# Performance work log

Hardware: AMD Instinct MI355X
Metric: run time of the kernel (lower is better)

## Reference

```python
import jax, jax.numpy as jnp
import numpy as np

_HMT = np.array([[1, 1, 1, 1], [1, -1, 1, -1], [1, 1, -1, -1], [1, -1, -1, 1]], dtype=np.float32)
_H = jnp.asarray(_HMT)
_H2 = jnp.asarray(_HMT[[1, 0, 2, 3], :])
_H3 = jnp.asarray(_HMT[[3, 1, 2, 0], :])
# inverse-transform rows 1:3 (2x4), reconstructed from truncated source
_IH = _H[1:3, :]
_IH2 = _H2[1:3, :]
_IH3 = _H3[1:3, :]

KERNEL = 4
STRIDE = 2


def setup_inputs() -> dict:
    key = jax.random.key(0)
    k1, k2, k3 = jax.random.split(key, 3)
    B, Cin, Cout, ih, iw = 16, 64, 96, 128, 128
    x = jax.random.normal(k1, (B, Cin, ih, iw), dtype=jnp.float32)
    weight = jax.random.normal(k2, (Cout, Cin, KERNEL, KERNEL), dtype=jnp.float32) * 0.05
    bias = jax.random.normal(k3, (1, Cout, 1, 1), dtype=jnp.float32) * 0.05
    return {"x": x, "weight": weight, "bias": bias}


def _extract_patches(xp, nH, nW):
    # patches[b,c,i,j,u,v] = xp[b,c, 2i+v, 2j+u]  (torch unfold(3).unfold(2) order)
    idx_h = 2 * np.arange(nH)[:, None] + np.arange(KERNEL)[None, :]  # (nH,4) over (i,v)
    idx_w = 2 * np.arange(nW)[:, None] + np.arange(KERNEL)[None, :]  # (nW,4) over (j,u)
    return xp[:, :, idx_h[:, None, None, :], idx_w[None, :, :, None]]  # (B,C,nH,nW,4,4)


def _group(t, w, ih_mat):
    # t: (B,C,nH,nW,4,4) transform-domain patches; w: (Og,C,4,4)
    m = jnp.einsum('bcijuv,ocuv->boijuv', t, w)
    # IH @ m @ IH.T -> (B,Og,nH,nW,2,2)
    return jnp.einsum('pu,boijuv,qv->boijpq', ih_mat, m, ih_mat)


def reference(x, weight, bias):
    B, Cin, ih, iw = x.shape
    Cout = weight.shape[0]
    nH, nW = ih // STRIDE, iw // STRIDE
    xp = jnp.pad(x, ((0, 0), (0, 0), (1, 1), (1, 1)))
    patches = _extract_patches(xp, nH, nW)
    # forward transforms: H @ P @ H ; H2.T @ P @ H2 ; H3.T @ P @ H3
    t1 = jnp.einsum('au,bcijuv,vd->bcijad', _H, patches, _H)
    t2 = jnp.einsum('ua,bcijuv,vd->bcijad', _H2, patches, _H2)
    t3 = jnp.einsum('ua,bcijuv,vd->bcijad', _H3, patches, _H3)
    g = Cout // 3
    h1 = _group(t1, weight[:g], _IH)
    h2 = _group(t2, weight[g:2 * g], _IH2)
    h3 = _group(t3, weight[2 * g:], _IH3)
    hmult = jnp.concatenate([h1, h2, h3], axis=1)  # (B,Cout,nH,nW,2,2)
    # out[b,o,2i+p,2j+q] = hmult[b,o,i,j,p,q]
    out = hmult.transpose(0, 1, 2, 4, 3, 5).reshape(B, Cout, ih, iw)
    return out + bias
```

## Files before the change

### kernel.cpp

```cpp
#include <hip/hip_runtime.h>
#include <hip/hip_bf16.h>
#include <cstddef>
#include <cstdint>


#define IHW 128
#define CIN 64
#define COUT 96
#define NCK 32
#define XB_DW 816
#define AB_DW 2048

typedef __attribute__((ext_vector_type(8))) short short8_t;
typedef __attribute__((ext_vector_type(4))) float floatx4;

__device__ __forceinline__ short bf16r(float f) {
  uint32_t u = __float_as_uint(f);
  uint32_t r = (u + 0x7FFFu + ((u >> 16) & 1u)) >> 16;
  return (short)r;
}

__device__ __forceinline__ uint32_t pk(float lo, float hi) {
  union { __hip_bfloat16 h; unsigned short s; } a, bq;
  a.h = __float2bfloat16(lo);
  bq.h = __float2bfloat16(hi);
  return (uint32_t)a.s | ((uint32_t)bq.s << 16);
}

__global__ __launch_bounds__(256) void prep_all(const float* __restrict__ x,
                                                const float* __restrict__ w,
                                                uint32_t* __restrict__ img,
                                                short* __restrict__ keff,
                                                int do_img) {
  if (blockIdx.x < 24) {
    int idx = blockIdx.x * 256 + threadIdx.x;
    if (idx >= COUT * CIN) return;
    int o = idx / CIN, c = idx % CIN;
    int g = o / 32;

    int perm[4] = {0, 1, 2, 3};
    if (g == 1) { perm[0] = 1; perm[1] = 0; }
    else if (g == 2) { perm[0] = 3; perm[3] = 0; }

    const float H[4][4] = {{1,1,1,1},{1,-1,1,-1},{1,1,-1,-1},{1,-1,-1,1}};
    float S[2][4];
#pragma unroll
    for (int p = 0; p < 2; ++p)
#pragma unroll
      for (int a = 0; a < 4; ++a) {
        bool pos = (g == 1) ? ((p == 0) ? true : (a < 2))
                            : ((p == 0) ? ((a & 1) == 0) : (a < 2));
        S[p][a] = pos ? 1.f : -1.f;
      }

    float wv[4][4];
#pragma unroll
    for (int a = 0; a < 4; ++a)
#pragma unroll
      for (int d = 0; d < 4; ++d) wv[a][d] = w[(o * CIN + c) * 16 + a * 4 + d];

    for (int p = 0; p < 2; ++p)
      for (int q = 0; q < 2; ++q) {
        int n = o * 4 + p * 2 + q;
        for (int y = 0; y < 4; ++y)
          for (int xx = 0; xx < 4; ++xx) {
            float s = 0.f;
#pragma unroll
            for (int a = 0; a < 4; ++a) {
              float ea = S[p][a] * H[a][perm[xx]];
#pragma unroll
              for (int d = 0; d < 4; ++d) s += ea * S[q][d] * H[d][perm[y]] * wv[a][d];
            }
            keff[n * 1024 + c * 16 + y * 4 + xx] = bf16r(s);
          }
      }
    return;
  }
  if (!do_img) return;

  const int t = (blockIdx.x - 24) * 256 + threadIdx.x;
  const int r = t >> 5;
  const int l = t & 31;
  const int py = r % 130;
  const int rc = r / 130;

  uint32_t d0 = 0, d1 = 0, t0 = 0;
  if (py != 0 && py != 129) {
    const float4 v = *reinterpret_cast<const float4*>(
        x + ((size_t)rc * IHW + (py - 1)) * IHW + 4 * l);
    float prev = __shfl_up(v.w, 1, 32);
    if (l == 0) prev = 0.f;
    d0 = pk(prev, v.x);
    d1 = pk(v.y, v.z);
    t0 = pk(v.w, 0.f);
  }
  uint32_t* row = img + (size_t)r * 68;
  *reinterpret_cast<uint2*>(row + 2 * l) = make_uint2(d0, d1);
  if (l == 31) *reinterpret_cast<uint4*>(row + 64) = make_uint4(t0, 0, 0, 0);
}

__global__ __launch_bounds__(256) void conv_mfma(const uint32_t* __restrict__ img,
                                                 const short* __restrict__ keff,
                                                 const float* __restrict__ bias,
                                                 float* __restrict__ out) {
  __shared__ uint32_t alds[4 * AB_DW];
  __shared__ uint32_t xlds[4 * XB_DW];

  const int tid = threadIdx.x;
  const int lane = tid & 63;
  const int wid = tid >> 6;
  const int wavem = wid >> 1;
  const int wn = wid & 1;
  const int l15 = lane & 15;
  const int l4 = lane >> 4;

  const int hw = blockIdx.x;
  const int xcd = hw & 7;
  const int r = hw >> 3;
  const int tile = xcd * 64 + r / 3;
  const int nblk = r % 3;
  const int b = tile >> 5;
  const int ib = tile & 31;

  const uint32_t* imgb = img + (size_t)b * CIN * 130 * 68;

  int xsrc = 0;
  const bool xact = tid < 204;
  {
    const int ri = tid / 17;
    const int col16 = tid % 17;
    const int y = ri >> 1;
    const int cs = ri & 1;
    xsrc = (cs * 130 + 4 * ib + y) * 68 + col16 * 4;
  }

  int asrc[2];
#pragma unroll
  for (int it = 0; it < 2; ++it) {
    const int slot = tid + it * 256;
    const int n = slot >> 2;
    const int p = slot & 3;
    asrc[it] = (nblk * 128 + n) * 1024 + ((p ^ ((n >> 1) & 3)) << 3);
  }

#define STAGE(bs, ckv)                                                     \
  {                                                                        \
    _Pragma("unroll") for (int it = 0; it < 2; ++it) {                     \
      const short* src = keff + asrc[it] + (ckv) * 32;                     \
      __builtin_amdgcn_global_load_lds(                                    \
          (const __attribute__((address_space(1))) void*)src,              \
          (__attribute__((address_space(3))) void*)                        \
              &alds[(bs) * AB_DW + (tid + it * 256) * 4],                  \
          16, 0, 0);                                                       \
    }                                                                      \
    if (xact) {                                                            \
      const uint32_t* src = imgb + xsrc + (ckv) * (2 * 130 * 68);          \
      __builtin_amdgcn_global_load_lds(                                    \
          (const __attribute__((address_space(1))) void*)src,              \
          (__attribute__((address_space(3))) void*)                        \
              &xlds[(bs) * XB_DW + tid * 4],                               \
          16, 0, 0);                                                       \
    }                                                                      \
  }

  union ufrag { short8_t s8; uint32_t u[4]; };

  floatx4 acc[4][4];
#pragma unroll
  for (int i2 = 0; i2 < 4; ++i2)
#pragma unroll
    for (int j2 = 0; j2 < 4; ++j2) acc[i2][j2] = (floatx4){0.f, 0.f, 0.f, 0.f};

  float biasr[4];
#pragma unroll
  for (int nf = 0; nf < 4; ++nf) biasr[nf] = bias[nblk * 32 + wn * 16 + nf * 4 + l4];

  const int abase = (wn * 64 + l15) * 16 + ((l4 ^ ((l15 >> 1) & 3)) << 2);
  const int xbase = (4 * wavem + 4 * (l4 & 1) + (l4 >> 1)) * 68 + l15;

#define COMPUTE(ckv)                                                       \
  {                                                                        \
    const uint32_t* Ap = alds + ((ckv) & 3) * AB_DW;                       \
    const uint32_t* Xp = xlds + ((ckv) & 3) * XB_DW + xbase;               \
    short8_t af[4];                                                        \
    _Pragma("unroll") for (int nf = 0; nf < 4; ++nf)                       \
      af[nf] = *reinterpret_cast<const short8_t*>(Ap + abase + nf * 256);  \
    ufrag xf[4];                                                           \
    _Pragma("unroll") for (int mf = 0; mf < 4; ++mf) {                     \
      const int o = mf * 16;                                               \
      xf[mf].u[0] = Xp[o];                                                 \
      xf[mf].u[1] = Xp[o + 1];                                             \
      xf[mf].u[2] = Xp[o + 136];                                           \
      xf[mf].u[3] = Xp[o + 137];                                           \
    }                                                                      \
    _Pragma("unroll") for (int mf = 0; mf < 4; ++mf)                       \
      _Pragma("unroll") for (int nf = 0; nf < 4; ++nf)                     \
        acc[mf][nf] = __builtin_amdgcn_mfma_f32_16x16x32_bf16(             \
            af[nf], xf[mf].s8, acc[mf][nf], 0, 0, 0);                      \
  }

  STAGE(0, 0);
  __builtin_amdgcn_sched_barrier(0);
  STAGE(1, 1);
  __builtin_amdgcn_sched_barrier(0);

  for (int ck = 0; ck < NCK - 2; ++ck) {
    STAGE((ck + 2) & 3, ck + 2);
    asm volatile("s_waitcnt vmcnt(6)" ::: "memory");
    __builtin_amdgcn_s_barrier();
    __builtin_amdgcn_sched_barrier(0);
    COMPUTE(ck);
  }
  asm volatile("s_waitcnt vmcnt(3)" ::: "memory");
  __builtin_amdgcn_s_barrier();
  __builtin_amdgcn_sched_barrier(0);
  COMPUTE(NCK - 2);
  asm volatile("s_waitcnt vmcnt(0)" ::: "memory");
  __builtin_amdgcn_s_barrier();
  __builtin_amdgcn_sched_barrier(0);
  COMPUTE(NCK - 1);

  const int i_row = ib * 2 + wavem;
  const int orow0 = 2 * i_row;
#pragma unroll
  for (int nf = 0; nf < 4; ++nf) {
    const int o = nblk * 32 + wn * 16 + nf * 4 + l4;
    const float bv = biasr[nf];
    float* obase = out + ((size_t)(b * COUT + o) * IHW + orow0) * IHW;
#pragma unroll
    for (int mf = 0; mf < 4; ++mf) {
      const int col = 2 * (mf * 16 + l15);
      float2 s0 = make_float2(acc[mf][nf][0] + bv, acc[mf][nf][1] + bv);
      float2 s1 = make_float2(acc[mf][nf][2] + bv, acc[mf][nf][3] + bv);
      *reinterpret_cast<float2*>(obase + col) = s0;
      *reinterpret_cast<float2*>(obase + IHW + col) = s1;
    }
  }
#undef STAGE
#undef COMPUTE
}

#define FB_P_DW 168
#define FB_COFF 80
#define FB_XBUF (12 * FB_P_DW)
#define FB_ABUF 4096

__global__ __launch_bounds__(256) void conv_fb(const float* __restrict__ x,
                                               const short* __restrict__ keff,
                                               const float* __restrict__ bias,
                                               float* __restrict__ out) {
  __shared__ uint32_t xlds[2 * FB_XBUF];
  __shared__ uint32_t alds[2 * FB_ABUF];

  const int tid = threadIdx.x;
  const int lane = tid & 63;
  const int wid = tid >> 6;
  const int wavem = wid >> 1;
  const int wn = wid & 1;
  const int l15 = lane & 15;
  const int l4 = lane >> 4;

  const int hw = blockIdx.x;
  const int xcd = hw & 7;
  const int r = hw >> 3;
  const int tile = xcd * 64 + r / 3;
  const int nblk = r % 3;
  const int b = tile >> 5;
  const int ib = tile & 31;
  const int gy0 = ib * 4 - 1;

  const float* xb = x + (size_t)b * CIN * IHW * IHW;

  int sl_off[3], sl_dw[3], sl_s[3];
  bool sl_ok[3];
#pragma unroll
  for (int it = 0; it < 3; ++it) {
    const int slot = tid + it * 256;
    const int seg = slot >> 5;
    const int s = slot & 31;
    const int c_sub = seg / 12;
    const int rr = seg % 12;
    const int kk2 = rr / 6;
    const int y = rr % 6;
    const int c_loc = 2 * kk2 + c_sub;
    const int gy = gy0 + y;
    const bool ok = (unsigned)gy < (unsigned)IHW;
    sl_off[it] = (c_loc * IHW + (ok ? gy : 0)) * IHW + 4 * s;
    sl_dw[it] = rr * FB_P_DW + c_sub * FB_COFF;
    sl_s[it] = s;
    sl_ok[it] = ok;
  }

  int aoff[4];
#pragma unroll
  for (int it = 0; it < 4; ++it) {
    const int slot = tid + it * 256;
    const int n = slot >> 3;
    const int u = slot & 7;
    aoff[it] = (nblk * 128 + n) * 1024 + ((u ^ (n & 7)) << 3);
  }

  float4 gv[3];
  float gn[3];
#define FISSUE(ckv)                                                       \
  {                                                                       \
    _Pragma("unroll") for (int it = 0; it < 3; ++it) {                    \
      const float* p = xb + sl_off[it] + (size_t)(ckv) * (4 * IHW * IHW); \
      gv[it] = *reinterpret_cast<const float4*>(p);                       \
      gn[it] = (sl_s[it] < 31) ? p[4] : 0.f;                              \
    }                                                                     \
  }
#define FWRITE(bs)                                                        \
  {                                                                       \
    uint32_t* Bp = xlds + (bs) * FB_XBUF;                                 \
    _Pragma("unroll") for (int it = 0; it < 3; ++it) {                    \
      float4 v = gv[it];                                                  \
      float nx = gn[it];                                                  \
      if (!sl_ok[it]) { v.x = 0.f; v.y = 0.f; v.z = 0.f; v.w = 0.f; nx = 0.f; } \
      const int o = sl_dw[it] + 2 * sl_s[it] + 1;                         \
      Bp[o] = pk(v.y, v.z);                                               \
      Bp[o + 1] = pk(v.w, nx);                                            \
      if (sl_s[it] == 0) Bp[sl_dw[it]] = pk(0.f, v.x);                    \
    }                                                                     \
  }
#define FADMA(bs, ckv)                                                    \
  {                                                                       \
    _Pragma("unroll") for (int it = 0; it < 4; ++it) {                    \
      const short* src = keff + aoff[it] + (ckv) * 64;                    \
      __builtin_amdgcn_global_load_lds(                                   \
          (const __attribute__((address_space(1))) void*)src,             \
          (__attribute__((address_space(3))) void*)                       \
              &alds[(bs) * FB_ABUF + (tid + it * 256) * 4],               \
          16, 0, 0);                                                      \
    }                                                                     \
  }

  union ufragf { short8_t s8; uint32_t u[4]; };
#define FKK(Apt, Xkt, abasev)                                             \
  {                                                                       \
    short8_t af[4];                                                       \
    _Pragma("unroll") for (int nf = 0; nf < 4; ++nf)                      \
      af[nf] = *reinterpret_cast<const short8_t*>((Apt) + (abasev) + nf * 512); \
    ufragf xf[4];                                                         \
    _Pragma("unroll") for (int mf = 0; mf < 4; ++mf) {                    \
      xf[mf].u[0] = (Xkt)[mf * 16];                                       \
      xf[mf].u[1] = (Xkt)[mf * 16 + 1];                                   \
      xf[mf].u[2] = (Xkt)[mf * 16 + FB_P_DW];                             \
      xf[mf].u[3] = (Xkt)[mf * 16 + FB_P_DW + 1];                         \
    }                                                                     \
    _Pragma("unroll") for (int mf = 0; mf < 4; ++mf)                      \
      _Pragma("unroll") for (int nf = 0; nf < 4; ++nf)                    \
        acc[mf][nf] = __builtin_amdgcn_mfma_f32_16x16x32_bf16(            \
            af[nf], xf[mf].s8, acc[mf][nf], 0, 0, 0);                     \
  }

  floatx4 acc[4][4];
#pragma unroll
  for (int i2 = 0; i2 < 4; ++i2)
#pragma unroll
    for (int j2 = 0; j2 < 4; ++j2) acc[i2][j2] = (floatx4){0.f, 0.f, 0.f, 0.f};

  float biasr[4];
#pragma unroll
  for (int nf = 0; nf < 4; ++nf) biasr[nf] = bias[nblk * 32 + wn * 16 + nf * 4 + l4];

  const int cm_dw = (2 * wavem + 2 * (l4 & 1)) * FB_P_DW + (l4 >> 1) * FB_COFF + l15;
  const int a0 = (wn * 64 + l15) * 32 + ((l4 ^ (l15 & 7)) << 2);
  const int a1 = a0 ^ 16;

  FISSUE(0);
  FADMA(0, 0);
  FWRITE(0);
  FISSUE(1);

  for (int ck = 0; ck < 16 - 1; ++ck) {
    asm volatile("s_waitcnt vmcnt(6) lgkmcnt(0)" ::: "memory");
    __builtin_amdgcn_s_barrier();
    __builtin_amdgcn_sched_barrier(0);
    const int cur = ck & 1;
    const uint32_t* Ap = alds + cur * FB_ABUF;
    const uint32_t* Xk0 = xlds + cur * FB_XBUF + cm_dw;
    const uint32_t* Xk1 = Xk0 + 6 * FB_P_DW;
    FADMA(cur ^ 1, ck + 1);
    FKK(Ap, Xk0, a0);
    FKK(Ap, Xk1, a1);
    FWRITE(cur ^ 1);
    if (ck + 2 < 16) FISSUE(ck + 2);
  }
  asm volatile("s_waitcnt vmcnt(0) lgkmcnt(0)" ::: "memory");
  __builtin_amdgcn_s_barrier();
  __builtin_amdgcn_sched_barrier(0);
  {
    const uint32_t* Ap = alds + FB_ABUF;
    const uint32_t* Xk0 = xlds + FB_XBUF + cm_dw;
    const uint32_t* Xk1 = Xk0 + 6 * FB_P_DW;
    FKK(Ap, Xk0, a0);
    FKK(Ap, Xk1, a1);
  }

  const int i_row = ib * 2 + wavem;
  const int orow0 = 2 * i_row;
#pragma unroll
  for (int nf = 0; nf < 4; ++nf) {
    const int o = nblk * 32 + wn * 16 + nf * 4 + l4;
    const float bv = biasr[nf];
    float* obase = out + ((size_t)(b * COUT + o) * IHW + orow0) * IHW;
#pragma unroll
    for (int mf = 0; mf < 4; ++mf) {
      const int col = 2 * (mf * 16 + l15);
      float2 s0 = make_float2(acc[mf][nf][0] + bv, acc[mf][nf][1] + bv);
      float2 s1 = make_float2(acc[mf][nf][2] + bv, acc[mf][nf][3] + bv);
      *reinterpret_cast<float2*>(obase + col) = s0;
      *reinterpret_cast<float2*>(obase + IHW + col) = s1;
    }
  }
#undef FISSUE
#undef FWRITE
#undef FADMA
#undef FKK
}

extern "C" void kernel_launch(void* const* d_in, const int* in_sizes, int n_in,
                              void* d_out, int out_size, void* d_ws, size_t ws_size,
                              hipStream_t stream) {
  const float* x = (const float*)d_in[0];
  const float* w = (const float*)d_in[1];
  const float* bias = (const float*)d_in[2];
  float* out = (float*)d_out;
  short* keff = (short*)d_ws;
  uint32_t* img = (uint32_t*)((char*)d_ws + 786432);

  const size_t NEED = 786432 + (size_t)16 * 64 * 130 * 272;
  const bool big = ws_size >= NEED;

  hipLaunchKernelGGL(prep_all, dim3(big ? 16664 : 24), dim3(256), 0, stream,
                     x, w, img, keff, big ? 1 : 0);
  if (big) {
    hipLaunchKernelGGL(conv_mfma, dim3(1536), dim3(256), 0, stream, img, keff, bias, out);
  } else {
    hipLaunchKernelGGL(conv_fb, dim3(1536), dim3(256), 0, stream, x, keff, bias, out);
  }
}
```

Measured before the change: 86.15 us.

## Load weight fragments directly into registers with double-buffered prefetch

The weight (A) operand is no longer staged through LDS with async global-to-LDS copies. Each wave now loads its MFMA weight fragments straight from global memory into registers, alternating between two register buffers. The main loop is unrolled by two and the vmcnt waits are adjusted to the new per-stage load counts. This frees 32 KB of LDS per block and removes the LDS reads for A, which may raise occupancy. The cost is that waves sharing the same weights each fetch them separately, with strided, less coalesced global loads and higher register pressure.

```diff
diff --git a/kernel.cpp b/kernel.cpp
--- a/kernel.cpp
+++ b/kernel.cpp
@@ -9,7 +9,6 @@
 #define COUT 96
 #define NCK 32
 #define XB_DW 816
-#define AB_DW 2048
 
 typedef __attribute__((ext_vector_type(8))) short short8_t;
 typedef __attribute__((ext_vector_type(4))) float floatx4;
@@ -103,7 +102,6 @@
                                                  const short* __restrict__ keff,
                                                  const float* __restrict__ bias,
                                                  float* __restrict__ out) {
-  __shared__ uint32_t alds[4 * AB_DW];
   __shared__ uint32_t xlds[4 * XB_DW];
 
   const int tid = threadIdx.x;
@@ -134,25 +132,8 @@
     xsrc = (cs * 130 + 4 * ib + y) * 68 + col16 * 4;
   }
 
-  int asrc[2];
-#pragma unroll
-  for (int it = 0; it < 2; ++it) {
-    const int slot = tid + it * 256;
-    const int n = slot >> 2;
-    const int p = slot & 3;
-    asrc[it] = (nblk * 128 + n) * 1024 + ((p ^ ((n >> 1) & 3)) << 3);
-  }
-
-#define STAGE(bs, ckv)                                                     \
+#define XSTAGE(bs, ckv)                                                    \
   {                                                                        \
-    _Pragma("unroll") for (int it = 0; it < 2; ++it) {                     \
-      const short* src = keff + asrc[it] + (ckv) * 32;                     \
-      __builtin_amdgcn_global_load_lds(                                    \
-          (const __attribute__((address_space(1))) void*)src,              \
-          (__attribute__((address_space(3))) void*)                        \
-              &alds[(bs) * AB_DW + (tid + it * 256) * 4],                  \
-          16, 0, 0);                                                       \
-    }                                                                      \
     if (xact) {                                                            \
       const uint32_t* src = imgb + xsrc + (ckv) * (2 * 130 * 68);          \
       __builtin_amdgcn_global_load_lds(                                    \
@@ -163,6 +144,14 @@
     }                                                                      \
   }
 
+  const short* aptr = keff + ((size_t)(nblk * 128 + wn * 64 + l15)) * 1024 + l4 * 8;
+
+#define ALOAD(af, ckv)                                                     \
+  {                                                                        \
+    _Pragma("unroll") for (int nf = 0; nf < 4; ++nf)                       \
+      af[nf] = *reinterpret_cast<const short8_t*>(aptr + nf * 16384 + (ckv) * 32); \
+  }
+
   union ufrag { short8_t s8; uint32_t u[4]; };
 
   floatx4 acc[4][4];
@@ -175,16 +164,11 @@
 #pragma unroll
   for (int nf = 0; nf < 4; ++nf) biasr[nf] = bias[nblk * 32 + wn * 16 + nf * 4 + l4];
 
-  const int abase = (wn * 64 + l15) * 16 + ((l4 ^ ((l15 >> 1) & 3)) << 2);
   const int xbase = (4 * wavem + 4 * (l4 & 1) + (l4 >> 1)) * 68 + l15;
 
-#define COMPUTE(ckv)                                                       \
+#define COMPUTE(ckv, af)                                                   \
   {                                                                        \
-    const uint32_t* Ap = alds + ((ckv) & 3) * AB_DW;                       \
     const uint32_t* Xp = xlds + ((ckv) & 3) * XB_DW + xbase;               \
-    short8_t af[4];                                                        \
-    _Pragma("unroll") for (int nf = 0; nf < 4; ++nf)                       \
-      af[nf] = *reinterpret_cast<const short8_t*>(Ap + abase + nf * 256);  \
     ufrag xf[4];                                                           \
     _Pragma("unroll") for (int mf = 0; mf < 4; ++mf) {                     \
       const int o = mf * 16;                                               \
@@ -199,26 +183,45 @@
             af[nf], xf[mf].s8, acc[mf][nf], 0, 0, 0);                      \
   }
 
-  STAGE(0, 0);
-  __builtin_amdgcn_sched_barrier(0);
-  STAGE(1, 1);
-  __builtin_amdgcn_sched_barrier(0);
-
-  for (int ck = 0; ck < NCK - 2; ++ck) {
-    STAGE((ck + 2) & 3, ck + 2);
+  short8_t afA[4], afB[4];
+
+  XSTAGE(0, 0);
+  __builtin_amdgcn_sched_barrier(0);
+  ALOAD(afA, 0);
+  __builtin_amdgcn_sched_barrier(0);
+  XSTAGE(1, 1);
+  __builtin_amdgcn_sched_barrier(0);
+  ALOAD(afB, 1);
+  __builtin_amdgcn_sched_barrier(0);
+
+  for (int ck = 0; ck < NCK - 2; ck += 2) {
+    XSTAGE((ck + 2) & 3, ck + 2);
     asm volatile("s_waitcnt vmcnt(6)" ::: "memory");
     __builtin_amdgcn_s_barrier();
     __builtin_amdgcn_sched_barrier(0);
-    COMPUTE(ck);
-  }
-  asm volatile("s_waitcnt vmcnt(3)" ::: "memory");
+    COMPUTE(ck, afA);
+    __builtin_amdgcn_sched_barrier(0);
+    ALOAD(afA, ck + 2);
+    __builtin_amdgcn_sched_barrier(0);
+
+    XSTAGE((ck + 3) & 3, ck + 3);
+    asm volatile("s_waitcnt vmcnt(6)" ::: "memory");
+    __builtin_amdgcn_s_barrier();
+    __builtin_amdgcn_sched_barrier(0);
+    COMPUTE(ck + 1, afB);
+    __builtin_amdgcn_sched_barrier(0);
+    ALOAD(afB, ck + 3);
+    __builtin_amdgcn_sched_barrier(0);
+  }
+
+  asm volatile("s_waitcnt vmcnt(5)" ::: "memory");
   __builtin_amdgcn_s_barrier();
   __builtin_amdgcn_sched_barrier(0);
-  COMPUTE(NCK - 2);
+  COMPUTE(NCK - 2, afA);
   asm volatile("s_waitcnt vmcnt(0)" ::: "memory");
   __builtin_amdgcn_s_barrier();
   __builtin_amdgcn_sched_barrier(0);
-  COMPUTE(NCK - 1);
+  COMPUTE(NCK - 1, afB);
 
   const int i_row = ib * 2 + wavem;
   const int orow0 = 2 * i_row;
@@ -236,7 +239,8 @@
       *reinterpret_cast<float2*>(obase + IHW + col) = s1;
     }
   }
-#undef STAGE
+#undef XSTAGE
+#undef ALOAD
 #undef COMPUTE
 }
 
@@ -329,7 +333,7 @@
       const short* src = keff + aoff[it] + (ckv) * 64;                    \
       __builtin_amdgcn_global_load_lds(                                   \
           (const __attribute__((address_space(1))) void*)src,             \
-          (__attribute__((address_space(3))) void*)                       \
+          (__attribute__((address_space(3))) void*)                      \
               &alds[(bs) * FB_ABUF + (tid + it * 256) * 4],               \
           16, 0, 0);                                                      \
     }                                                                     \
```

New measurement: 131.7 us. 1.53x slower.
